# Optimization experiments

Measured on AMD Instinct MI355X. Metric: run time of the kernel, lower is better.

## Reference

```python
import jax, jax.numpy as jnp
import numpy as np

TEMP = 0.1  # simclr_temp


def setup_inputs() -> dict:
    key = jax.random.key(0)
    features = jax.random.normal(key, (4096, 512), dtype=jnp.float32)
    return {"features": features}


def reference(features):
    N, d = features.shape
    B = N // 2

    # L2-normalize rows (torch F.normalize, eps=1e-12)
    norm = jnp.maximum(jnp.linalg.norm(features, axis=1, keepdims=True), 1e-12)
    f = features / norm

    # dense cosine-similarity matrix [N, N]
    sim = f @ f.T

    # static index bookkeeping (numpy, known at trace time)
    idx = np.arange(N)
    pos_col = (idx + B) % N  # the other view of the same image

    # positives: sim[i, (i+B) % N], shape [N, 1]
    pos = sim[jnp.arange(N), jnp.asarray(pos_col)][:, None]

    # negatives: all columns except the diagonal and the positive, ascending
    # order per row, exactly matching torch's ~mask .view reshapes -> [N, N-2]
    full = np.broadcast_to(idx, (N, N))
    keep = (full != idx[:, None]) & (full != pos_col[:, None])
    neg_cols = jnp.asarray(full[keep].reshape(N, N - 2))
    neg = jnp.take_along_axis(sim, neg_cols, axis=1)

    logits = jnp.concatenate([pos, neg], axis=1) / TEMP  # [N, N-1]

    # cross-entropy with target class 0 for every row
    loss = jnp.mean(jax.nn.logsumexp(logits, axis=1) - logits[:, 0])
    return loss
```

## Files before the change

### kernel.cpp

```cpp
#include <hip/hip_runtime.h>
#include <hip/hip_bf16.h>

typedef unsigned short u16;
typedef __attribute__((ext_vector_type(8))) short short8;
typedef __attribute__((ext_vector_type(4))) float f32x4;

#define NROWS 4096
#define DIM   512
#define TINV  10.0f

__device__ __forceinline__ u16 f2bf(float x) {
    unsigned u = __float_as_uint(x);
    unsigned r = (u + 0x7FFFu + ((u >> 16) & 1u)) >> 16;
    return (u16)r;
}

__global__ __launch_bounds__(256) void k_norm(const float* __restrict__ in,
                                              u16* __restrict__ out,
                                              float* __restrict__ S) {
    const int row  = blockIdx.x * 4 + (threadIdx.x >> 6);
    const int lane = threadIdx.x & 63;
    if (threadIdx.x < 4) S[blockIdx.x * 4 + threadIdx.x] = 0.f;

    const float* rp = in + (size_t)row * DIM;
    float4 v0 = ((const float4*)rp)[lane];
    float4 v1 = ((const float4*)rp)[lane + 64];

    float ssq = v0.x*v0.x + v0.y*v0.y + v0.z*v0.z + v0.w*v0.w
              + v1.x*v1.x + v1.y*v1.y + v1.z*v1.z + v1.w*v1.w;
    #pragma unroll
    for (int m = 32; m; m >>= 1) ssq += __shfl_xor(ssq, m);

    const float scale = 1.0f / fmaxf(sqrtf(ssq), 1e-12f);

    u16* op = out + (size_t)row * DIM;
    ((ushort4*)op)[lane] = make_ushort4(
        f2bf(v0.x * scale), f2bf(v0.y * scale),
        f2bf(v0.z * scale), f2bf(v0.w * scale));
    ((ushort4*)op)[lane + 64] = make_ushort4(
        f2bf(v1.x * scale), f2bf(v1.y * scale),
        f2bf(v1.z * scale), f2bf(v1.w * scale));
}

__device__ __forceinline__ void gload_lds16(const u16* g, u16* l) {
    __builtin_amdgcn_global_load_lds(
        (const __attribute__((address_space(1))) void*)g,
        (__attribute__((address_space(3))) void*)l, 16, 0, 0);
}

__global__ __launch_bounds__(256) void k_gemm(const u16* __restrict__ fb,
                                              float* __restrict__ S,
                                              float* __restrict__ P) {
    const int br = blockIdx.y, bc = blockIdx.x;
    if (bc < br) return;
    const bool diag = (br == bc);
    const bool posT = (bc == (br ^ 16));

    __shared__ u16 lA[128 * 64];
    __shared__ u16 lB[128 * 64];

    const int tid  = threadIdx.x;
    const int lane = tid & 63;
    const int wid  = tid >> 6;
    const int wr   = wid >> 1;
    const int wc   = wid & 1;
    const int brow = br * 128;
    const int bcol = bc * 128;
    const int lr   = lane & 15;
    const int kg   = lane >> 4;

    f32x4 acc[4][4];
    #pragma unroll
    for (int m = 0; m < 4; ++m)
        #pragma unroll
        for (int n = 0; n < 4; ++n)
            acc[m][n] = (f32x4){0.f, 0.f, 0.f, 0.f};

    const u16* Bsrc = diag ? lA : lB;

    for (int kk = 0; kk < DIM; kk += 64) {
        #pragma unroll
        for (int i = 0; i < 4; ++i) {
            const int q  = tid + i * 256;
            const int r  = q >> 3;
            const int c  = q & 7;
            const int sc = c ^ (r & 7);
            gload_lds16(fb + (size_t)(brow + r) * DIM + kk + sc * 8, lA + q * 8);
        }
        if (!diag) {
            #pragma unroll
            for (int i = 0; i < 4; ++i) {
                const int q  = tid + i * 256;
                const int r  = q >> 3;
                const int c  = q & 7;
                const int sc = c ^ (r & 7);
                gload_lds16(fb + (size_t)(bcol + r) * DIM + kk + sc * 8, lB + q * 8);
            }
        }
        __syncthreads();

        short8 a[4][2], b[4][2];
        #pragma unroll
        for (int m = 0; m < 4; ++m) {
            const int row = wr * 64 + m * 16 + lr;
            #pragma unroll
            for (int ks = 0; ks < 2; ++ks)
                a[m][ks] = *(const short8*)
                    &lA[row * 64 + (((ks * 4 + kg) ^ (row & 7)) * 8)];
        }
        #pragma unroll
        for (int n = 0; n < 4; ++n) {
            const int row = wc * 64 + n * 16 + lr;
            #pragma unroll
            for (int ks = 0; ks < 2; ++ks)
                b[n][ks] = *(const short8*)
                    &Bsrc[row * 64 + (((ks * 4 + kg) ^ (row & 7)) * 8)];
        }

        #pragma unroll
        for (int ks = 0; ks < 2; ++ks)
            #pragma unroll
            for (int m = 0; m < 4; ++m)
                #pragma unroll
                for (int n = 0; n < 4; ++n)
                    acc[m][n] = __builtin_amdgcn_mfma_f32_16x16x32_bf16(
                        a[m][ks], b[n][ks], acc[m][n], 0, 0, 0);
        __syncthreads();
    }

    float cs[4] = {0.f, 0.f, 0.f, 0.f};
    #pragma unroll
    for (int m = 0; m < 4; ++m) {
        #pragma unroll
        for (int r = 0; r < 4; ++r) {
            const int grow = brow + wr * 64 + m * 16 + kg * 4 + r;
            float rs = 0.f;
            #pragma unroll
            for (int n = 0; n < 4; ++n) {
                const int gcol = bcol + wc * 64 + n * 16 + lr;
                const float s = acc[m][n][r];
                if (posT && gcol == (grow ^ 2048)) { P[grow] = s; P[gcol] = s; }
                float e = __expf(TINV * (s - 1.0f));
                if (diag && gcol == grow) e = 0.f;
                rs += e;
                if (!diag) cs[n] += e;
            }
            rs += __shfl_xor(rs, 1);
            rs += __shfl_xor(rs, 2);
            rs += __shfl_xor(rs, 4);
            rs += __shfl_xor(rs, 8);
            if (lr == 0) atomicAdd(&S[grow], rs);
        }
    }
    if (!diag) {
        #pragma unroll
        for (int n = 0; n < 4; ++n) {
            cs[n] += __shfl_xor(cs[n], 16);
            cs[n] += __shfl_xor(cs[n], 32);
            if (kg == 0)
                atomicAdd(&S[bcol + wc * 64 + n * 16 + lr], cs[n]);
        }
    }
}

__global__ __launch_bounds__(1024) void k_final(const float* __restrict__ S,
                                                const float* __restrict__ P,
                                                float* __restrict__ out) {
    __shared__ float red[1024];
    float local = 0.f;
    #pragma unroll
    for (int i = 0; i < 4; ++i) {
        const int r = threadIdx.x + i * 1024;
        local += TINV + logf(S[r]) - TINV * P[r];
    }
    red[threadIdx.x] = local;
    __syncthreads();
    #pragma unroll
    for (int s = 512; s; s >>= 1) {
        if (threadIdx.x < s) red[threadIdx.x] += red[threadIdx.x + s];
        __syncthreads();
    }
    if (threadIdx.x == 0) out[0] = red[0] * (1.0f / NROWS);
}

extern "C" void kernel_launch(void* const* d_in, const int* in_sizes, int n_in,
                              void* d_out, int out_size, void* d_ws, size_t ws_size,
                              hipStream_t stream) {
    const float* feat = (const float*)d_in[0];

    u16*   fb = (u16*)d_ws;
    float* S  = (float*)((char*)d_ws + (size_t)NROWS * DIM * 2);
    float* P  = S + NROWS;

    k_norm<<<NROWS / 4, 256, 0, stream>>>(feat, fb, S);
    k_gemm<<<dim3(32, 32), 256, 0, stream>>>(fb, S, P);
    k_final<<<1, 1024, 0, stream>>>(S, P, (float*)d_out);
}
```

Baseline: 88.95 us.

## Fuse final reduction into GEMM via last-block counter and compact triangular grid

Launches only the 528 upper-triangular tiles with a closed-form index mapping, so 496 blocks no longer start only to exit. Folds the final log-sum reduction into the GEMM kernel: every block bumps an atomic counter after a fence, and the last block reads S and P and writes the loss. This drops one kernel launch and the idle early-exit blocks. In exchange it adds a fence and an atomic per block, and the final reduction runs serially in a single 256-thread block.

Measured after the change: 119.6 us. 1.34x slower.

```diff
diff --git a/kernel.cpp b/kernel.cpp
--- a/kernel.cpp
+++ b/kernel.cpp
@@ -8,6 +8,8 @@
 #define NROWS 4096
 #define DIM   512
 #define TINV  10.0f
+#define NTILE 32
+#define NBLK  528
 
 __device__ __forceinline__ u16 f2bf(float x) {
     unsigned u = __float_as_uint(x);
@@ -17,10 +19,12 @@
 
 __global__ __launch_bounds__(256) void k_norm(const float* __restrict__ in,
                                               u16* __restrict__ out,
-                                              float* __restrict__ S) {
+                                              float* __restrict__ S,
+                                              unsigned* __restrict__ ctr) {
     const int row  = blockIdx.x * 4 + (threadIdx.x >> 6);
     const int lane = threadIdx.x & 63;
     if (threadIdx.x < 4) S[blockIdx.x * 4 + threadIdx.x] = 0.f;
+    if (blockIdx.x == 0 && threadIdx.x == 0) *ctr = 0u;
 
     const float* rp = in + (size_t)row * DIM;
     float4 v0 = ((const float4*)rp)[lane];
@@ -50,14 +54,23 @@
 
 __global__ __launch_bounds__(256) void k_gemm(const u16* __restrict__ fb,
                                               float* __restrict__ S,
-                                              float* __restrict__ P) {
-    const int br = blockIdx.y, bc = blockIdx.x;
-    if (bc < br) return;
+                                              float* __restrict__ P,
+                                              unsigned* __restrict__ ctr,
+                                              float* __restrict__ out) {
+    const int t = blockIdx.x;
+    int br = (int)((65.0f - sqrtf(4225.0f - 8.0f * (float)t)) * 0.5f);
+    br = br < 0 ? 0 : (br > 31 ? 31 : br);
+    while (br * (65 - br) / 2 > t) --br;
+    while ((br + 1) * (64 - br) / 2 <= t) ++br;
+    const int bc = br + (t - br * (65 - br) / 2);
+
     const bool diag = (br == bc);
     const bool posT = (bc == (br ^ 16));
 
     __shared__ u16 lA[128 * 64];
     __shared__ u16 lB[128 * 64];
+    __shared__ unsigned s_done;
+    __shared__ float red[4];
 
     const int tid  = threadIdx.x;
     const int lane = tid & 63;
@@ -161,26 +174,31 @@
                 atomicAdd(&S[bcol + wc * 64 + n * 16 + lr], cs[n]);
         }
     }
-}
-
-__global__ __launch_bounds__(1024) void k_final(const float* __restrict__ S,
-                                                const float* __restrict__ P,
-                                                float* __restrict__ out) {
-    __shared__ float red[1024];
+
+    __threadfence();
+    __syncthreads();
+    if (tid == 0) {
+        unsigned old = atomicAdd(ctr, 1u);
+        s_done = (old == NBLK - 1u);
+    }
+    __syncthreads();
+    if (!s_done) return;
+    __threadfence();
+
     float local = 0.f;
-    #pragma unroll
-    for (int i = 0; i < 4; ++i) {
-        const int r = threadIdx.x + i * 1024;
-        local += TINV + logf(S[r]) - TINV * P[r];
-    }
-    red[threadIdx.x] = local;
+    for (int r = tid; r < NROWS; r += 256) {
+        float Sv = __hip_atomic_load(&S[r], __ATOMIC_RELAXED,
+                                     __HIP_MEMORY_SCOPE_AGENT);
+        float Pv = __hip_atomic_load(&P[r], __ATOMIC_RELAXED,
+                                     __HIP_MEMORY_SCOPE_AGENT);
+        local += TINV + logf(Sv) - TINV * Pv;
+    }
+    #pragma unroll
+    for (int m = 32; m; m >>= 1) local += __shfl_xor(local, m);
+    if (lane == 0) red[wid] = local;
     __syncthreads();
-    #pragma unroll
-    for (int s = 512; s; s >>= 1) {
-        if (threadIdx.x < s) red[threadIdx.x] += red[threadIdx.x + s];
-        __syncthreads();
-    }
-    if (threadIdx.x == 0) out[0] = red[0] * (1.0f / NROWS);
+    if (tid == 0)
+        out[0] = (red[0] + red[1] + red[2] + red[3]) * (1.0f / NROWS);
 }
 
 extern "C" void kernel_launch(void* const* d_in, const int* in_sizes, int n_in,
@@ -188,11 +206,11 @@
                               hipStream_t stream) {
     const float* feat = (const float*)d_in[0];
 
-    u16*   fb = (u16*)d_ws;
-    float* S  = (float*)((char*)d_ws + (size_t)NROWS * DIM * 2);
-    float* P  = S + NROWS;
-
-    k_norm<<<NROWS / 4, 256, 0, stream>>>(feat, fb, S);
-    k_gemm<<<dim3(32, 32), 256, 0, stream>>>(fb, S, P);
-    k_final<<<1, 1024, 0, stream>>>(S, P, (float*)d_out);
-}
+    u16*      fb  = (u16*)d_ws;
+    float*    S   = (float*)((char*)d_ws + (size_t)NROWS * DIM * 2);
+    float*    P   = S + NROWS;
+    unsigned* ctr = (unsigned*)(P + NROWS);
+
+    k_norm<<<NROWS / 4, 256, 0, stream>>>(feat, fb, S, ctr);
+    k_gemm<<<NBLK, 256, 0, stream>>>(fb, S, P, ctr, (float*)d_out);
+}
```

## Use per-wave 64x64 triangular tiles with direct global fragment loads

Applied to the files above, without the earlier changes.

Replaces the 128x128 block tiling, which used LDS staging and launched a full 32x32 grid that discarded lower-triangle blocks, with independent per-wave 64x64 tiles. Only the 2080 upper-triangle tiles are enumerated, decoded from a linear index via a sqrt formula and spread across blocks with a swizzle. MFMA operand fragments are loaded straight from global memory into registers, so LDS and __syncthreads are no longer used. This removes idle blocks and barrier overhead, but each wave now gets less data reuse and relies on L2 and the cache for repeated row reads.

Measured after the change: 114.0 us. 28.1% more time.

```diff
diff --git a/kernel.cpp b/kernel.cpp
--- a/kernel.cpp
+++ b/kernel.cpp
@@ -8,6 +8,9 @@
 #define NROWS 4096
 #define DIM   512
 #define TINV  10.0f
+#define NTILE 64
+#define NT    2080
+#define NBLK  520
 
 __device__ __forceinline__ u16 f2bf(float x) {
     unsigned u = __float_as_uint(x);
@@ -42,32 +45,29 @@
         f2bf(v1.z * scale), f2bf(v1.w * scale));
 }
 
-__device__ __forceinline__ void gload_lds16(const u16* g, u16* l) {
-    __builtin_amdgcn_global_load_lds(
-        (const __attribute__((address_space(1))) void*)g,
-        (__attribute__((address_space(3))) void*)l, 16, 0, 0);
-}
-
 __global__ __launch_bounds__(256) void k_gemm(const u16* __restrict__ fb,
                                               float* __restrict__ S,
                                               float* __restrict__ P) {
-    const int br = blockIdx.y, bc = blockIdx.x;
-    if (bc < br) return;
+    const int swz = (blockIdx.x & 7) * (NBLK / 8) + (blockIdx.x >> 3);
+    const int t   = swz * 4 + (threadIdx.x >> 6);
+
+    int br = (int)((129.0f - sqrtf(16641.0f - 8.0f * (float)t)) * 0.5f);
+    br = br < 0 ? 0 : (br > 63 ? 63 : br);
+    while (br * (129 - br) / 2 > t) --br;
+    while ((br + 1) * (128 - br) / 2 <= t) ++br;
+    const int bc = br + (t - br * (129 - br) / 2);
+
     const bool diag = (br == bc);
-    const bool posT = (bc == (br ^ 16));
+    const bool posT = (bc == (br ^ 32));
 
-    __shared__ u16 lA[128 * 64];
-    __shared__ u16 lB[128 * 64];
-
-    const int tid  = threadIdx.x;
-    const int lane = tid & 63;
-    const int wid  = tid >> 6;
-    const int wr   = wid >> 1;
-    const int wc   = wid & 1;
-    const int brow = br * 128;
-    const int bcol = bc * 128;
+    const int lane = threadIdx.x & 63;
     const int lr   = lane & 15;
     const int kg   = lane >> 4;
+    const int brow = br * 64;
+    const int bcol = bc * 64;
+
+    const u16* pa = fb + (size_t)(brow + lr) * DIM + kg * 8;
+    const u16* pb = fb + (size_t)(bcol + lr) * DIM + kg * 8;
 
     f32x4 acc[4][4];
     #pragma unroll
@@ -76,56 +76,37 @@
         for (int n = 0; n < 4; ++n)
             acc[m][n] = (f32x4){0.f, 0.f, 0.f, 0.f};
 
-    const u16* Bsrc = diag ? lA : lB;
-
-    for (int kk = 0; kk < DIM; kk += 64) {
-        #pragma unroll
-        for (int i = 0; i < 4; ++i) {
-            const int q  = tid + i * 256;
-            const int r  = q >> 3;
-            const int c  = q & 7;
-            const int sc = c ^ (r & 7);
-            gload_lds16(fb + (size_t)(brow + r) * DIM + kk + sc * 8, lA + q * 8);
-        }
-        if (!diag) {
+    if (diag) {
+        #pragma unroll 4
+        for (int kk = 0; kk < DIM; kk += 32) {
+            short8 a[4];
             #pragma unroll
-            for (int i = 0; i < 4; ++i) {
-                const int q  = tid + i * 256;
-                const int r  = q >> 3;
-                const int c  = q & 7;
-                const int sc = c ^ (r & 7);
-                gload_lds16(fb + (size_t)(bcol + r) * DIM + kk + sc * 8, lB + q * 8);
-            }
-        }
-        __syncthreads();
-
-        short8 a[4][2], b[4][2];
-        #pragma unroll
-        for (int m = 0; m < 4; ++m) {
-            const int row = wr * 64 + m * 16 + lr;
-            #pragma unroll
-            for (int ks = 0; ks < 2; ++ks)
-                a[m][ks] = *(const short8*)
-                    &lA[row * 64 + (((ks * 4 + kg) ^ (row & 7)) * 8)];
-        }
-        #pragma unroll
-        for (int n = 0; n < 4; ++n) {
-            const int row = wc * 64 + n * 16 + lr;
-            #pragma unroll
-            for (int ks = 0; ks < 2; ++ks)
-                b[n][ks] = *(const short8*)
-                    &Bsrc[row * 64 + (((ks * 4 + kg) ^ (row & 7)) * 8)];
-        }
-
-        #pragma unroll
-        for (int ks = 0; ks < 2; ++ks)
+            for (int m = 0; m < 4; ++m)
+                a[m] = *(const short8*)(pa + (size_t)(m * 16) * DIM + kk);
             #pragma unroll
             for (int m = 0; m < 4; ++m)
                 #pragma unroll
                 for (int n = 0; n < 4; ++n)
                     acc[m][n] = __builtin_amdgcn_mfma_f32_16x16x32_bf16(
-                        a[m][ks], b[n][ks], acc[m][n], 0, 0, 0);
-        __syncthreads();
+                        a[m], a[n], acc[m][n], 0, 0, 0);
+        }
+    } else {
+        #pragma unroll 4
+        for (int kk = 0; kk < DIM; kk += 32) {
+            short8 a[4], b[4];
+            #pragma unroll
+            for (int m = 0; m < 4; ++m)
+                a[m] = *(const short8*)(pa + (size_t)(m * 16) * DIM + kk);
+            #pragma unroll
+            for (int n = 0; n < 4; ++n)
+                b[n] = *(const short8*)(pb + (size_t)(n * 16) * DIM + kk);
+            #pragma unroll
+            for (int m = 0; m < 4; ++m)
+                #pragma unroll
+                for (int n = 0; n < 4; ++n)
+                    acc[m][n] = __builtin_amdgcn_mfma_f32_16x16x32_bf16(
+                        a[m], b[n], acc[m][n], 0, 0, 0);
+        }
     }
 
     float cs[4] = {0.f, 0.f, 0.f, 0.f};
@@ -133,11 +114,11 @@
     for (int m = 0; m < 4; ++m) {
         #pragma unroll
         for (int r = 0; r < 4; ++r) {
-            const int grow = brow + wr * 64 + m * 16 + kg * 4 + r;
+            const int grow = brow + m * 16 + kg * 4 + r;
             float rs = 0.f;
             #pragma unroll
             for (int n = 0; n < 4; ++n) {
-                const int gcol = bcol + wc * 64 + n * 16 + lr;
+                const int gcol = bcol + n * 16 + lr;
                 const float s = acc[m][n][r];
                 if (posT && gcol == (grow ^ 2048)) { P[grow] = s; P[gcol] = s; }
                 float e = __expf(TINV * (s - 1.0f));
@@ -158,7 +139,7 @@
             cs[n] += __shfl_xor(cs[n], 16);
             cs[n] += __shfl_xor(cs[n], 32);
             if (kg == 0)
-                atomicAdd(&S[bcol + wc * 64 + n * 16 + lr], cs[n]);
+                atomicAdd(&S[bcol + n * 16 + lr], cs[n]);
         }
     }
 }
@@ -193,6 +174,6 @@
     float* P  = S + NROWS;
 
     k_norm<<<NROWS / 4, 256, 0, stream>>>(feat, fb, S);
-    k_gemm<<<dim3(32, 32), 256, 0, stream>>>(fb, S, P);
+    k_gemm<<<NBLK, 256, 0, stream>>>(fb, S, P);
     k_final<<<1, 1024, 0, stream>>>(S, P, (float*)d_out);
 }
```

## Keep full A row-panel in LDS, stream double-buffered B tiles over column group

Applied to the files above, without the earlier changes.

The GEMM moves from a triangular 32x32 grid of 128x128 tiles to 256 blocks. Each block loads a full 128x512 A panel into LDS once, then streams four 128-column B tiles through a double-buffered LDS pipeline, with row exp-sums kept in registers. Symmetry exploitation (upper-triangle only plus column sums) is dropped, so the matrix-multiply work roughly doubles. In exchange it removes idle blocks, reloads of A and column atomics, and overlaps B loads with compute, at the cost of 160KB LDS per block and low occupancy.

New measurement: 94.22 us. 5.9% more time.

```diff
diff --git a/kernel.cpp b/kernel.cpp
--- a/kernel.cpp
+++ b/kernel.cpp
@@ -48,117 +48,150 @@
         (__attribute__((address_space(3))) void*)l, 16, 0, 0);
 }
 
+#define LDS_A_ELEMS (128 * 512)
+#define LDS_B_ELEMS (128 * 64)
+#define LDS_BYTES   ((LDS_A_ELEMS + 2 * LDS_B_ELEMS) * 2)
+
 __global__ __launch_bounds__(256) void k_gemm(const u16* __restrict__ fb,
                                               float* __restrict__ S,
                                               float* __restrict__ P) {
-    const int br = blockIdx.y, bc = blockIdx.x;
-    if (bc < br) return;
-    const bool diag = (br == bc);
-    const bool posT = (bc == (br ^ 16));
-
-    __shared__ u16 lA[128 * 64];
-    __shared__ u16 lB[128 * 64];
+    extern __shared__ u16 lds[];
+    u16* lA  = lds;
+    u16* lB0 = lds + LDS_A_ELEMS;
+    u16* lB1 = lds + LDS_A_ELEMS + LDS_B_ELEMS;
+
+    const int br  = blockIdx.x >> 3;
+    const int bcg = blockIdx.x & 7;
 
     const int tid  = threadIdx.x;
     const int lane = tid & 63;
     const int wid  = tid >> 6;
     const int wr   = wid >> 1;
     const int wc   = wid & 1;
-    const int brow = br * 128;
-    const int bcol = bc * 128;
     const int lr   = lane & 15;
     const int kg   = lane >> 4;
 
-    f32x4 acc[4][4];
+    const u16* Abase = fb + (size_t)(br * 128) * DIM;
+    const u16* Bbase = fb + (size_t)(bcg * 512) * DIM;
+
+    #pragma unroll
+    for (int i = 0; i < 32; ++i) {
+        const int q  = tid + i * 256;
+        const int r  = q >> 6;
+        const int c  = q & 63;
+        const int sc = c ^ (r & 7);
+        gload_lds16(Abase + (size_t)r * DIM + sc * 8, lA + q * 8);
+    }
+    #pragma unroll
+    for (int i = 0; i < 4; ++i) {
+        const int q  = tid + i * 256;
+        const int r  = q >> 3;
+        const int c  = q & 7;
+        const int sc = c ^ (r & 7);
+        gload_lds16(Bbase + (size_t)r * DIM + sc * 8, lB0 + q * 8);
+    }
+    __syncthreads();
+
+    float rsum[4][4];
     #pragma unroll
     for (int m = 0; m < 4; ++m)
         #pragma unroll
-        for (int n = 0; n < 4; ++n)
-            acc[m][n] = (f32x4){0.f, 0.f, 0.f, 0.f};
-
-    const u16* Bsrc = diag ? lA : lB;
-
-    for (int kk = 0; kk < DIM; kk += 64) {
-        #pragma unroll
-        for (int i = 0; i < 4; ++i) {
-            const int q  = tid + i * 256;
-            const int r  = q >> 3;
-            const int c  = q & 7;
-            const int sc = c ^ (r & 7);
-            gload_lds16(fb + (size_t)(brow + r) * DIM + kk + sc * 8, lA + q * 8);
+        for (int r = 0; r < 4; ++r) rsum[m][r] = 0.f;
+
+    #pragma unroll 1
+    for (int bct = 0; bct < 4; ++bct) {
+        f32x4 acc[4][4];
+        #pragma unroll
+        for (int m = 0; m < 4; ++m)
+            #pragma unroll
+            for (int n = 0; n < 4; ++n)
+                acc[m][n] = (f32x4){0.f, 0.f, 0.f, 0.f};
+
+        #pragma unroll 1
+        for (int k8 = 0; k8 < 8; ++k8) {
+            const int s = bct * 8 + k8;
+            if (s < 31) {
+                const int sn   = s + 1;
+                const int bctn = sn >> 3;
+                const int kkn  = (sn & 7) * 64;
+                u16* dst = (sn & 1) ? lB1 : lB0;
+                #pragma unroll
+                for (int i = 0; i < 4; ++i) {
+                    const int q  = tid + i * 256;
+                    const int r  = q >> 3;
+                    const int c  = q & 7;
+                    const int sc = c ^ (r & 7);
+                    gload_lds16(Bbase + (size_t)(bctn * 128 + r) * DIM + kkn + sc * 8,
+                                dst + q * 8);
+                }
+            }
+            const int kk = k8 * 64;
+            const u16* bbuf = (s & 1) ? lB1 : lB0;
+            short8 a[4][2], b[4][2];
+            #pragma unroll
+            for (int m = 0; m < 4; ++m) {
+                const int row = wr * 64 + m * 16 + lr;
+                #pragma unroll
+                for (int ks = 0; ks < 2; ++ks) {
+                    const int kc = (kk >> 3) + ks * 4 + kg;
+                    a[m][ks] = *(const short8*)
+                        &lA[(row * 64 + (kc ^ (row & 7))) * 8];
+                }
+            }
+            #pragma unroll
+            for (int n = 0; n < 4; ++n) {
+                const int row = wc * 64 + n * 16 + lr;
+                #pragma unroll
+                for (int ks = 0; ks < 2; ++ks) {
+                    const int kc = ks * 4 + kg;
+                    b[n][ks] = *(const short8*)
+                        &bbuf[(row * 8 + (kc ^ (row & 7))) * 8];
+                }
+            }
+            #pragma unroll
+            for (int ks = 0; ks < 2; ++ks)
+                #pragma unroll
+                for (int m = 0; m < 4; ++m)
+                    #pragma unroll
+                    for (int n = 0; n < 4; ++n)
+                        acc[m][n] = __builtin_amdgcn_mfma_f32_16x16x32_bf16(
+                            a[m][ks], b[n][ks], acc[m][n], 0, 0, 0);
+            __syncthreads();
         }
-        if (!diag) {
-            #pragma unroll
-            for (int i = 0; i < 4; ++i) {
-                const int q  = tid + i * 256;
-                const int r  = q >> 3;
-                const int c  = q & 7;
-                const int sc = c ^ (r & 7);
-                gload_lds16(fb + (size_t)(bcol + r) * DIM + kk + sc * 8, lB + q * 8);
+
+        const int bc_abs = bcg * 4 + bct;
+        const bool posT  = (bc_abs == (br ^ 16));
+        #pragma unroll
+        for (int m = 0; m < 4; ++m) {
+            #pragma unroll
+            for (int r = 0; r < 4; ++r) {
+                const int grow = br * 128 + wr * 64 + m * 16 + kg * 4 + r;
+                #pragma unroll
+                for (int n = 0; n < 4; ++n) {
+                    const int gcol = bc_abs * 128 + wc * 64 + n * 16 + lr;
+                    const float sv = acc[m][n][r];
+                    if (posT && gcol == (grow ^ 2048)) P[grow] = sv;
+                    float e = __expf(TINV * (sv - 1.0f));
+                    if (gcol == grow) e = 0.f;
+                    rsum[m][r] += e;
+                }
             }
         }
-        __syncthreads();
-
-        short8 a[4][2], b[4][2];
-        #pragma unroll
-        for (int m = 0; m < 4; ++m) {
-            const int row = wr * 64 + m * 16 + lr;
-            #pragma unroll
-            for (int ks = 0; ks < 2; ++ks)
-                a[m][ks] = *(const short8*)
-                    &lA[row * 64 + (((ks * 4 + kg) ^ (row & 7)) * 8)];
-        }
-        #pragma unroll
-        for (int n = 0; n < 4; ++n) {
-            const int row = wc * 64 + n * 16 + lr;
-            #pragma unroll
-            for (int ks = 0; ks < 2; ++ks)
-                b[n][ks] = *(const short8*)
-                    &Bsrc[row * 64 + (((ks * 4 + kg) ^ (row & 7)) * 8)];
-        }
-
-        #pragma unroll
-        for (int ks = 0; ks < 2; ++ks)
-            #pragma unroll
-            for (int m = 0; m < 4; ++m)
-                #pragma unroll
-                for (int n = 0; n < 4; ++n)
-                    acc[m][n] = __builtin_amdgcn_mfma_f32_16x16x32_bf16(
-                        a[m][ks], b[n][ks], acc[m][n], 0, 0, 0);
-        __syncthreads();
-    }
-
-    float cs[4] = {0.f, 0.f, 0.f, 0.f};
+    }
+
     #pragma unroll
     for (int m = 0; m < 4; ++m) {
         #pragma unroll
         for (int r = 0; r < 4; ++r) {
-            const int grow = brow + wr * 64 + m * 16 + kg * 4 + r;
-            float rs = 0.f;
-            #pragma unroll
-            for (int n = 0; n < 4; ++n) {
-                const int gcol = bcol + wc * 64 + n * 16 + lr;
-                const float s = acc[m][n][r];
-                if (posT && gcol == (grow ^ 2048)) { P[grow] = s; P[gcol] = s; }
-                float e = __expf(TINV * (s - 1.0f));
-                if (diag && gcol == grow) e = 0.f;
-                rs += e;
-                if (!diag) cs[n] += e;
-            }
+            float rs = rsum[m][r];
             rs += __shfl_xor(rs, 1);
             rs += __shfl_xor(rs, 2);
             rs += __shfl_xor(rs, 4);
             rs += __shfl_xor(rs, 8);
-            if (lr == 0) atomicAdd(&S[grow], rs);
-        }
-    }
-    if (!diag) {
-        #pragma unroll
-        for (int n = 0; n < 4; ++n) {
-            cs[n] += __shfl_xor(cs[n], 16);
-            cs[n] += __shfl_xor(cs[n], 32);
-            if (kg == 0)
-                atomicAdd(&S[bcol + wc * 64 + n * 16 + lr], cs[n]);
+            if (lr == 0) {
+                const int grow = br * 128 + wr * 64 + m * 16 + kg * 4 + r;
+                atomicAdd(&S[grow], rs);
+            }
         }
     }
 }
@@ -192,7 +225,11 @@
     float* S  = (float*)((char*)d_ws + (size_t)NROWS * DIM * 2);
     float* P  = S + NROWS;
 
+    (void)hipFuncSetAttribute((const void*)k_gemm,
+                              hipFuncAttributeMaxDynamicSharedMemorySize,
+                              LDS_BYTES);
+
     k_norm<<<NROWS / 4, 256, 0, stream>>>(feat, fb, S);
-    k_gemm<<<dim3(32, 32), 256, 0, stream>>>(fb, S, P);
+    k_gemm<<<256, 256, LDS_BYTES, stream>>>(fb, S, P);
     k_final<<<1, 1024, 0, stream>>>(S, P, (float*)d_out);
 }
```
